# Optimization experiments

Measured on AMD Instinct MI355X. Metric: run time of the kernel, lower is better.

Reference implementation:

```python
import jax, jax.numpy as jnp
import numpy as np

NFEAT, NHID, NCLASS = 64, 64, 32
B, N_SOLUTE, N_SOLVENT = 2, 2076, 8940


def setup_inputs() -> dict:
    key = jax.random.key(0)
    ks = jax.random.split(key, 20)
    s = 0.05
    return {
        "solute_adj": jax.random.uniform(ks[0], (B, N_SOLUTE, N_SOLUTE), jnp.float32),
        "solute_meth": jax.random.normal(ks[1], (B, N_SOLUTE, NFEAT), jnp.float32),
        "solvent_meth": jax.random.normal(ks[2], (B, N_SOLVENT, NFEAT), jnp.float32),
        "solvent_adj_meth": jax.random.uniform(ks[3], (B, N_SOLVENT, N_SOLVENT), jnp.float32),
        "W_fc1": jax.random.normal(ks[4], (NFEAT, NCLASS), jnp.float32) * s,
        "b_fc1": jnp.zeros((NCLASS,), jnp.float32),
        "W_c1": jax.random.normal(ks[5], (NFEAT, NHID), jnp.float32) * s,
        "b_c1": jnp.zeros((NHID,), jnp.float32),
        "W_c2": jax.random.normal(ks[6], (NHID, NCLASS), jnp.float32) * s,
        "b_c2": jnp.zeros((NCLASS,), jnp.float32),
        "W_fc2": jax.random.normal(ks[7], (2 * NCLASS, NCLASS), jnp.float32) * s,
        "b_fc2": jnp.zeros((NCLASS,), jnp.float32),
        "W_fc3": jax.random.normal(ks[8], (NCLASS, 64), jnp.float32) * s,
        "b_fc3": jnp.zeros((64,), jnp.float32),
        "W_fc4": jax.random.normal(ks[9], (64, 32), jnp.float32) * s,
        "b_fc4": jnp.zeros((32,), jnp.float32),
        "W_fc5": jax.random.normal(ks[10], (32, 1), jnp.float32) * s,
        "b_fc5": jnp.zeros((1,), jnp.float32),
    }


def _branch(x, adj, W_fc1, b_fc1, W_c1, b_c1, W_c2, b_c2):
    # residual linear skip: fc1(x)
    init = x @ W_fc1 + b_fc1                          # [B, N, nclass]
    # GCNConv 1: adj @ (x W) + b, relu
    h = jax.nn.relu(jnp.einsum("bnm,bmh->bnh", adj, x @ W_c1) + b_c1)
    # GCNConv 2 + skip
    out = jnp.einsum("bnm,bmc->bnc", adj, h @ W_c2) + b_c2 + init  # [B, N, nclass]
    # global max pool: batch index is block-contiguous -> max over node axis
    return jnp.max(out, axis=1)                       # [B, nclass]


def reference(solute_adj, solute_meth, solvent_meth, solvent_adj_meth,
              W_fc1, b_fc1, W_c1, b_c1, W_c2, b_c2,
              W_fc2, b_fc2, W_fc3, b_fc3, W_fc4, b_fc4, W_fc5, b_fc5):
    su = _branch(solute_meth, solute_adj, W_fc1, b_fc1, W_c1, b_c1, W_c2, b_c2)
    sv = _branch(solvent_meth, solvent_adj_meth, W_fc1, b_fc1, W_c1, b_c1, W_c2, b_c2)
    d = jnp.concatenate([su, sv], axis=1)             # [B, 2*nclass]
    d = jax.nn.relu(d @ W_fc2 + b_fc2)                # dropout = identity (eval)
    d = jax.nn.relu(d @ W_fc3 + b_fc3)
    d = jax.nn.relu(d @ W_fc4 + b_fc4)
    return d @ W_fc5 + b_fc5                          # [B, 1]
```

## Files before the change

kernel.cpp:

```cpp
#include <hip/hip_runtime.h>

#define B_      2
#define NSU     2076
#define NSV     8940
#define ROWS_SU (B_ * NSU)
#define ROWS_ALL (B_ * (NSU + NSV))
#define NB64_SV 140
#define NB64_SU 33
#define NBX_TOT (2 * NB64_SV + 2 * NB64_SU)
#define NH2     8
#define NCH_SV  140
#define NCH_SU  33
#define TK_SV   140
#define TK_SU   33
#define T_SV    560
#define T_SU    132
#define TILES_TOT (2 * T_SV + 2 * T_SU)
#define PADROWS (TILES_TOT * 16)
#define TSZ8_SV ((size_t)140 * 1024)
#define TSZ8_SU ((size_t)34 * 1024)
#define SU_BASE8 ((size_t)2 * T_SV * TSZ8_SV)
#define PRE_BLKS ((ROWS_ALL + 255) / 256)
#define NEG_INF (-3.402823466e38f)

#define Y1F_SV(b) ((size_t)(b) * 140 * 4096)
#define Y1F_SU(b) ((size_t)2 * 140 * 4096 + (size_t)(b) * 34 * 4096)
#define Y2F8_SV(b) ((size_t)(b) * 140 * 2048)
#define Y2F8_SU(b) ((size_t)2 * 140 * 2048 + (size_t)(b) * 34 * 2048)

typedef __attribute__((ext_vector_type(8))) short bf16x8;
typedef __attribute__((ext_vector_type(4))) float f32x4;
typedef __attribute__((ext_vector_type(2))) long longx2;

#define MFMA16 __builtin_amdgcn_mfma_f32_16x16x32_bf16
#define MFMA8  __builtin_amdgcn_mfma_f32_16x16x32_fp8_fp8

__device__ __forceinline__ unsigned short f2bf(float x) {
    unsigned int u = __float_as_uint(x);
    u += 0x7FFFu + ((u >> 16) & 1u);
    return (unsigned short)(u >> 16);
}
__device__ __forceinline__ unsigned int pkbf(float lo, float hi) {
    unsigned int r;
    asm("v_cvt_pk_bf16_f32 %0, %1, %2" : "=v"(r) : "v"(lo), "v"(hi));
    return r;
}
__device__ __forceinline__ int pk8lo(float lo, float hi, int old) {
    return __builtin_amdgcn_cvt_pk_fp8_f32(lo, hi, old, false);
}
__device__ __forceinline__ int pk8hi(float lo, float hi, int old) {
    return __builtin_amdgcn_cvt_pk_fp8_f32(lo, hi, old, true);
}
__device__ __forceinline__ float bf2f(short s) {
    return __uint_as_float(((unsigned int)(unsigned short)s) << 16);
}

__global__ __launch_bounds__(256) void pre_kernel(
    const float* __restrict__ xsu, const float* __restrict__ xsv,
    const float* __restrict__ Wc1, const float* __restrict__ Wfc1,
    const float* __restrict__ bfc1, const float* __restrict__ Wc2g,
    unsigned short* __restrict__ y1tf, float* __restrict__ initb,
    unsigned short* __restrict__ wc2t)
{
    const int tid = threadIdx.x;
    if (blockIdx.x == PRE_BLKS) {
        for (int idx = tid; idx < 2048; idx += 256) {
            const int c = idx >> 6, f = idx & 63;
            wc2t[idx] = f2bf(Wc2g[f * 32 + c]);
        }
        return;
    }

    __shared__ float sWc1[64 * 64];
    __shared__ float sWfc1[64 * 32];
    __shared__ float sb[32];
    for (int i = tid; i < 64 * 64; i += 256) sWc1[i] = Wc1[i];
    for (int i = tid; i < 64 * 32; i += 256) sWfc1[i] = Wfc1[i];
    if (tid < 32) sb[tid] = bfc1[tid];
    __syncthreads();

    const int rid = blockIdx.x * 256 + tid;
    if (rid >= ROWS_ALL) return;

    const float* xrow; unsigned short* yb; int m;
    if (rid < ROWS_SU) {
        int b = rid / NSU; m = rid - b * NSU;
        xrow = xsu + (size_t)rid * 64;
        yb = y1tf + Y1F_SU(b);
    } else {
        int r2 = rid - ROWS_SU;
        int b = r2 / NSV; m = r2 - b * NSV;
        xrow = xsv + (size_t)r2 * 64;
        yb = y1tf + Y1F_SV(b);
    }

    float xr[64];
    #pragma unroll
    for (int f4 = 0; f4 < 16; ++f4) {
        float4 v = ((const float4*)xrow)[f4];
        xr[f4 * 4 + 0] = v.x; xr[f4 * 4 + 1] = v.y;
        xr[f4 * 4 + 2] = v.z; xr[f4 * 4 + 3] = v.w;
    }
    {
        const int chunk = m >> 6, half = (m >> 5) & 1, kqq = (m >> 3) & 3, e = m & 7;
        unsigned short* yw = yb + (size_t)chunk * 4096 + half * 512 + e;
        for (int c = 0; c < 64; ++c) {
            float acc = 0.f;
            #pragma unroll
            for (int f = 0; f < 64; ++f) acc += xr[f] * sWc1[f * 64 + c];
            yw[(c >> 4) * 1024 + ((c & 15) + 16 * kqq) * 8] = f2bf(acc);
        }
    }
    float* ini = initb + (size_t)rid * 32;
    for (int c = 0; c < 32; ++c) {
        float acc = sb[c];
        #pragma unroll
        for (int f = 0; f < 64; ++f) acc += xr[f] * sWfc1[f * 32 + c];
        ini[c] = acc;
    }
}

__global__ __launch_bounds__(256) void conv1f_kernel(
    const float* __restrict__ adj_su, const float* __restrict__ adj_sv,
    const unsigned short* __restrict__ y1tf,
    const float* __restrict__ bc1, const unsigned short* __restrict__ wc2t,
    unsigned char* __restrict__ abf8,
    unsigned char* __restrict__ y2f8)
{
    __shared__ unsigned short AL[4096];
    __shared__ unsigned short HL[1024];

    const int t = blockIdx.x;
    const int tid = threadIdx.x, lane = tid & 63, w = tid >> 6;
    const int l15 = lane & 15, kq = lane >> 4;

    int M, row0, TK;
    const float* A; const unsigned short* Yf;
    unsigned char* AbT; unsigned char* Y2b;
    if (t < 2 * T_SV) {
        int b = t / T_SV, rt = t - b * T_SV;
        M = NSV; TK = TK_SV;
        A = adj_sv + (size_t)b * NSV * NSV;
        Yf = y1tf + Y1F_SV(b);
        AbT = abf8 + (size_t)t * TSZ8_SV;
        Y2b = y2f8 + Y2F8_SV(b);
        row0 = rt * 16;
    } else {
        int u = t - 2 * T_SV;
        int b = u / T_SU, rt = u - b * T_SU;
        M = NSU; TK = TK_SU;
        A = adj_su + (size_t)b * NSU * NSU;
        Yf = y1tf + Y1F_SU(b);
        AbT = abf8 + SU_BASE8 + (size_t)u * TSZ8_SU;
        Y2b = y2f8 + Y2F8_SU(b);
        row0 = rt * 16;
    }

    const float* Ar[4];
    #pragma unroll
    for (int rr = 0; rr < 4; ++rr) {
        int r = row0 + w * 4 + rr;
        if (r >= M) r = M - 1;
        Ar[rr] = A + (size_t)r * M;
    }

    const int c4 = lane * 4;
    const int k64i = c4 >> 6;
    const int c63 = c4 & 63;
    const int rxor = (l15 & 7) << 3;

    f32x4 acc = {0.f, 0.f, 0.f, 0.f};

    for (int ch = 0; ch < TK; ch += 4) {
        const int cb = ch * 64;
        const int nk = (TK - ch < 4) ? (TK - ch) : 4;
        #pragma unroll
        for (int rr = 0; rr < 4; ++rr) {
            const int r = w * 4 + rr;
            const int col = cb + c4;
            float4 v = make_float4(0.f, 0.f, 0.f, 0.f);
            if (col < M) v = *(const float4*)(Ar[rr] + col);
            const unsigned int u0 = pkbf(v.x, v.y);
            const unsigned int u1 = pkbf(v.z, v.w);
            const int sa = k64i * 1024 + r * 64 + (c63 ^ ((r & 7) << 3));
            *(uint2*)(&AL[sa]) = make_uint2(u0, u1);
        }
        __syncthreads();
        #pragma unroll
        for (int j = 0; j < 4; ++j) {
            if (j < nk) {
                const bf16x8 af0 = *(const bf16x8*)(&AL[j * 1024 + l15 * 64 + ((kq * 8) ^ rxor)]);
                const bf16x8 af1 = *(const bf16x8*)(&AL[j * 1024 + l15 * 64 + ((32 + kq * 8) ^ rxor)]);
                const unsigned short* bb = Yf + (size_t)(ch + j) * 4096 + w * 1024 + lane * 8;
                const bf16x8 b0 = *(const bf16x8*)(bb);
                const bf16x8 b1 = *(const bf16x8*)(bb + 512);
                acc = MFMA16(af0, b0, acc, 0, 0, 0);
                acc = MFMA16(af1, b1, acc, 0, 0, 0);
            }
        }
        if (w < nk) {
            const bf16x8 h0 = *(const bf16x8*)(&AL[w * 1024 + l15 * 64 + ((kq * 8) ^ rxor)]);
            const bf16x8 h1 = *(const bf16x8*)(&AL[w * 1024 + l15 * 64 + ((32 + kq * 8) ^ rxor)]);
            int q0 = pk8lo(bf2f(h0[0]), bf2f(h0[1]), 0); q0 = pk8hi(bf2f(h0[2]), bf2f(h0[3]), q0);
            int q1 = pk8lo(bf2f(h0[4]), bf2f(h0[5]), 0); q1 = pk8hi(bf2f(h0[6]), bf2f(h0[7]), q1);
            int q2 = pk8lo(bf2f(h1[0]), bf2f(h1[1]), 0); q2 = pk8hi(bf2f(h1[2]), bf2f(h1[3]), q2);
            int q3 = pk8lo(bf2f(h1[4]), bf2f(h1[5]), 0); q3 = pk8hi(bf2f(h1[6]), bf2f(h1[7]), q3);
            *(int4*)(AbT + (size_t)(ch + w) * 1024 + lane * 16) = make_int4(q0, q1, q2, q3);
        }
        __syncthreads();
    }

    {
        const float bcv = bc1[w * 16 + l15];
        #pragma unroll
        for (int j = 0; j < 4; ++j) {
            const int r = kq * 4 + j;
            const int c = w * 16 + l15;
            HL[r * 64 + (c ^ ((r & 7) << 3))] = f2bf(fmaxf(acc[j] + bcv, 0.f));
        }
    }
    __syncthreads();
    if (w < 2) {
        const bf16x8 hf0 = *(const bf16x8*)(&HL[l15 * 64 + ((kq * 8) ^ rxor)]);
        const bf16x8 hf1 = *(const bf16x8*)(&HL[l15 * 64 + ((32 + kq * 8) ^ rxor)]);
        const unsigned short* wp = wc2t + (size_t)(w * 16 + l15) * 64 + kq * 8;
        const bf16x8 w0 = *(const bf16x8*)(wp);
        const bf16x8 w1 = *(const bf16x8*)(wp + 32);
        f32x4 m = {0.f, 0.f, 0.f, 0.f};
        m = MFMA16(hf0, w0, m, 0, 0, 0);
        m = MFMA16(hf1, w1, m, 0, 0, 0);
        const int mrow = row0 + kq * 4;
        const int chm = mrow >> 6, r6 = mrow & 63;
        const int halfm = r6 >> 5, kqqm = (r6 >> 3) & 3, e0 = r6 & 7;
        const int c = w * 16 + l15;
        int pk = pk8lo(m[0], m[1], 0); pk = pk8hi(m[2], m[3], pk);
        *(int*)(Y2b + (size_t)chm * 2048 + (c >> 4) * 1024
                + (kqqm * 16 + (c & 15)) * 16 + halfm * 8 + e0) = pk;
    }
}

__global__ __launch_bounds__(256) void conv2p_kernel(
    const unsigned char* __restrict__ abf8,
    const unsigned char* __restrict__ y2f8,
    float* __restrict__ p2)
{
    const int bid = (NBX_TOT - 1) - blockIdx.x;
    const int q = blockIdx.y;
    const int tid = threadIdx.x, lane = tid & 63, wid = tid >> 6;
    int tile0, cbeg, cend;
    const unsigned char* Yf2; const unsigned char* AbT;
    if (bid < 2 * NB64_SV) {
        int b = bid / NB64_SV, rb = bid - b * NB64_SV;
        Yf2 = y2f8 + Y2F8_SV(b);
        tile0 = b * T_SV + rb * 4;
        AbT = abf8 + (size_t)(tile0 + wid) * TSZ8_SV;
        cbeg = (q * NCH_SV) >> 3;
        cend = ((q + 1) * NCH_SV) >> 3;
    } else {
        int t = bid - 2 * NB64_SV;
        int b = t / NB64_SU, rb = t - b * NB64_SU;
        Yf2 = y2f8 + Y2F8_SU(b);
        int tsu = b * T_SU + rb * 4;
        tile0 = 2 * T_SV + tsu;
        AbT = abf8 + SU_BASE8 + (size_t)(tsu + wid) * TSZ8_SU;
        cbeg = (q * NCH_SU) >> 3;
        cend = ((q + 1) * NCH_SU) >> 3;
    }

    const int l15 = lane & 15, kq = lane >> 4;
    const unsigned char* Apl = AbT + (size_t)lane * 16;
    const unsigned char* Bpl = Yf2 + (size_t)lane * 16;

    f32x4 acc0 = {0.f,0.f,0.f,0.f}, acc1 = acc0;

    longx2 fa, fc;
    longx2 b0, b1, d0, d1;

#define LDA2(F, ch) do { F = *(const longx2*)(Apl + (size_t)(ch) * 1024); } while (0)
#define LDB2(B0,B1,ch) do { \
    const unsigned char* bb = Bpl + (size_t)(ch) * 2048; \
    B0 = *(const longx2*)(bb); \
    B1 = *(const longx2*)(bb + 1024); } while (0)
#define CMP4(F,B0,B1) do { \
    acc0 = MFMA8(F[0], B0[0], acc0, 0, 0, 0); \
    acc1 = MFMA8(F[0], B1[0], acc1, 0, 0, 0); \
    acc0 = MFMA8(F[1], B0[1], acc0, 0, 0, 0); \
    acc1 = MFMA8(F[1], B1[1], acc1, 0, 0, 0); } while (0)

    if (cbeg < cend) {
        LDA2(fa, cbeg);
        LDB2(b0, b1, cbeg);
        int ch = cbeg;
        while (ch + 2 <= cend) {
            LDA2(fc, ch + 1);
            LDB2(d0, d1, ch + 1);
            CMP4(fa, b0, b1);
            if (ch + 2 < cend) {
                LDA2(fa, ch + 2);
                LDB2(b0, b1, ch + 2);
            }
            CMP4(fc, d0, d1);
            ch += 2;
        }
        if (ch < cend) {
            CMP4(fa, b0, b1);
        }
    }
#undef LDA2
#undef LDB2
#undef CMP4

    float* Pp = p2 + ((size_t)q * TILES_TOT + tile0 + wid) * (16 * 32);
    #pragma unroll
    for (int j = 0; j < 4; ++j) {
        const int r = kq * 4 + j;
        Pp[r * 32 +      l15] = acc0[j];
        Pp[r * 32 + 16 + l15] = acc1[j];
    }
}

__global__ __launch_bounds__(256) void combine2_kernel(
    const float* __restrict__ p2, const float* __restrict__ bc2,
    const float* __restrict__ initb, float* __restrict__ part)
{
    const int idx = blockIdx.x * 256 + threadIdx.x;
    if (idx >= TILES_TOT * 32) return;
    const int gt = idx >> 5, c = idx & 31;
    int m0, M; const float* I;
    if (gt < 2 * T_SV) {
        int b = gt / T_SV;
        m0 = (gt - b * T_SV) * 16;
        M = NSV;
        I = initb + (size_t)ROWS_SU * 32 + (size_t)b * NSV * 32;
    } else {
        int t = gt - 2 * T_SV;
        int b = t / T_SU;
        m0 = (t - b * T_SU) * 16;
        M = NSU;
        I = initb + (size_t)b * NSU * 32;
    }
    const float* Q = p2 + (size_t)gt * 16 * 32 + c;
    const size_t QS = (size_t)TILES_TOT * 16 * 32;
    const float bb = bc2[c];
    float mx = NEG_INF;
    #pragma unroll
    for (int r = 0; r < 16; ++r) {
        const int m = m0 + r;
        if (m < M) {
            float s = bb + I[(size_t)m * 32 + c];
            #pragma unroll
            for (int qq = 0; qq < NH2; ++qq) s += Q[(size_t)qq * QS + r * 32];
            mx = fmaxf(mx, s);
        }
    }
    part[(size_t)gt * 32 + c] = mx;
}

__global__ __launch_bounds__(128) void head_kernel(
    const float* __restrict__ part,
    const float* __restrict__ Wfc2, const float* __restrict__ bfc2,
    const float* __restrict__ Wfc3, const float* __restrict__ bfc3,
    const float* __restrict__ Wfc4, const float* __restrict__ bfc4,
    const float* __restrict__ Wfc5, const float* __restrict__ bfc5,
    float* __restrict__ out)
{
    __shared__ float d[2][64];
    __shared__ float t1[2][32];
    __shared__ float t2[2][64];
    __shared__ float t3[2][32];
    const int tid = threadIdx.x;

    if (tid < 64) {
        const int b = tid >> 5, c = tid & 31;
        float m = NEG_INF;
        const float* ps = part + (size_t)(2 * T_SV + b * T_SU) * 32 + c;
        for (int i = 0; i < T_SU; ++i) m = fmaxf(m, ps[(size_t)i * 32]);
        d[b][c] = m;
        float m2 = NEG_INF;
        const float* pv = part + (size_t)b * T_SV * 32 + c;
        for (int i = 0; i < T_SV; ++i) m2 = fmaxf(m2, pv[(size_t)i * 32]);
        d[b][32 + c] = m2;
    }
    __syncthreads();
    if (tid < 64) {
        const int b = tid >> 5, c = tid & 31;
        float acc = bfc2[c];
        for (int f = 0; f < 64; ++f) acc += d[b][f] * Wfc2[f * 32 + c];
        t1[b][c] = fmaxf(acc, 0.f);
    }
    __syncthreads();
    {
        const int b = tid >> 6, c = tid & 63;
        float acc = bfc3[c];
        for (int f = 0; f < 32; ++f) acc += t1[b][f] * Wfc3[f * 64 + c];
        t2[b][c] = fmaxf(acc, 0.f);
    }
    __syncthreads();
    if (tid < 64) {
        const int b = tid >> 5, c = tid & 31;
        float acc = bfc4[c];
        for (int f = 0; f < 64; ++f) acc += t2[b][f] * Wfc4[f * 32 + c];
        t3[b][c] = fmaxf(acc, 0.f);
    }
    __syncthreads();
    if (tid < 2) {
        float acc = bfc5[0];
        for (int f = 0; f < 32; ++f) acc += t3[tid][f] * Wfc5[f];
        out[tid] = acc;
    }
}

extern "C" void kernel_launch(void* const* d_in, const int* in_sizes, int n_in,
                              void* d_out, int out_size, void* d_ws, size_t ws_size,
                              hipStream_t stream)
{
    const float* solute_adj   = (const float*)d_in[0];
    const float* solute_meth  = (const float*)d_in[1];
    const float* solvent_meth = (const float*)d_in[2];
    const float* solvent_adj  = (const float*)d_in[3];
    const float* W_fc1 = (const float*)d_in[4];
    const float* b_fc1 = (const float*)d_in[5];
    const float* W_c1  = (const float*)d_in[6];
    const float* b_c1  = (const float*)d_in[7];
    const float* W_c2  = (const float*)d_in[8];
    const float* b_c2  = (const float*)d_in[9];
    const float* W_fc2 = (const float*)d_in[10];
    const float* b_fc2 = (const float*)d_in[11];
    const float* W_fc3 = (const float*)d_in[12];
    const float* b_fc3 = (const float*)d_in[13];
    const float* W_fc4 = (const float*)d_in[14];
    const float* b_fc4 = (const float*)d_in[15];
    const float* W_fc5 = (const float*)d_in[16];
    const float* b_fc5 = (const float*)d_in[17];
    float* out = (float*)d_out;

    char* wsb = (char*)d_ws;
    size_t off = 0;
    unsigned short* y1tf = (unsigned short*)(wsb + off); off += 2850816;
    unsigned char*  y2f8 = (unsigned char*)(wsb + off);  off += 712704;
    unsigned short* wc2t = (unsigned short*)(wsb + off); off += 4096;
    float* initb         = (float*)(wsb + off);          off += 2820096;
    unsigned char* abf8  = (unsigned char*)(wsb + off);
    off += SU_BASE8 + (size_t)2 * T_SU * TSZ8_SU;
    off = (off + 15) & ~(size_t)15;
    float* p2            = (float*)(wsb + off);
    off += (size_t)NH2 * PADROWS * 32 * 4;
    float* part          = (float*)(wsb + off);          off += (size_t)TILES_TOT * 32 * 4;

    pre_kernel<<<dim3(PRE_BLKS + 1), dim3(256), 0, stream>>>(
        solute_meth, solvent_meth, W_c1, W_fc1, b_fc1, W_c2, y1tf, initb, wc2t);

    conv1f_kernel<<<dim3(TILES_TOT), dim3(256), 0, stream>>>(
        solute_adj, solvent_adj, y1tf, b_c1, wc2t, abf8, y2f8);

    conv2p_kernel<<<dim3(NBX_TOT, NH2), dim3(256), 0, stream>>>(abf8, y2f8, p2);

    combine2_kernel<<<dim3((TILES_TOT * 32 + 255) / 256), dim3(256), 0, stream>>>(
        p2, b_c2, initb, part);

    head_kernel<<<dim3(1), dim3(128), 0, stream>>>(
        part, W_fc2, b_fc2, W_fc3, b_fc3, W_fc4, b_fc4, W_fc5, b_fc5, out);
}
```

Baseline: 440.8 us.

## Double-buffer adjacency staging in conv1 and deepen conv2 fp8 load prefetch

```diff
diff --git a/kernel.cpp b/kernel.cpp
--- a/kernel.cpp
+++ b/kernel.cpp
@@ -127,7 +127,7 @@
     unsigned char* __restrict__ abf8,
     unsigned char* __restrict__ y2f8)
 {
-    __shared__ unsigned short AL[4096];
+    __shared__ unsigned short AL[2][4096];
     __shared__ unsigned short HL[1024];
 
     const int t = blockIdx.x;
@@ -170,46 +170,81 @@
     const int rxor = (l15 & 7) << 3;
 
     f32x4 acc = {0.f, 0.f, 0.f, 0.f};
-
-    for (int ch = 0; ch < TK; ch += 4) {
-        const int cb = ch * 64;
-        const int nk = (TK - ch < 4) ? (TK - ch) : 4;
-        #pragma unroll
-        for (int rr = 0; rr < 4; ++rr) {
-            const int r = w * 4 + rr;
-            const int col = cb + c4;
-            float4 v = make_float4(0.f, 0.f, 0.f, 0.f);
-            if (col < M) v = *(const float4*)(Ar[rr] + col);
-            const unsigned int u0 = pkbf(v.x, v.y);
-            const unsigned int u1 = pkbf(v.z, v.w);
-            const int sa = k64i * 1024 + r * 64 + (c63 ^ ((r & 7) << 3));
-            *(uint2*)(&AL[sa]) = make_uint2(u0, u1);
-        }
-        __syncthreads();
-        #pragma unroll
-        for (int j = 0; j < 4; ++j) {
-            if (j < nk) {
-                const bf16x8 af0 = *(const bf16x8*)(&AL[j * 1024 + l15 * 64 + ((kq * 8) ^ rxor)]);
-                const bf16x8 af1 = *(const bf16x8*)(&AL[j * 1024 + l15 * 64 + ((32 + kq * 8) ^ rxor)]);
-                const unsigned short* bb = Yf + (size_t)(ch + j) * 4096 + w * 1024 + lane * 8;
-                const bf16x8 b0 = *(const bf16x8*)(bb);
-                const bf16x8 b1 = *(const bf16x8*)(bb + 512);
-                acc = MFMA16(af0, b0, acc, 0, 0, 0);
-                acc = MFMA16(af1, b1, acc, 0, 0, 0);
-            }
-        }
-        if (w < nk) {
-            const bf16x8 h0 = *(const bf16x8*)(&AL[w * 1024 + l15 * 64 + ((kq * 8) ^ rxor)]);
-            const bf16x8 h1 = *(const bf16x8*)(&AL[w * 1024 + l15 * 64 + ((32 + kq * 8) ^ rxor)]);
-            int q0 = pk8lo(bf2f(h0[0]), bf2f(h0[1]), 0); q0 = pk8hi(bf2f(h0[2]), bf2f(h0[3]), q0);
-            int q1 = pk8lo(bf2f(h0[4]), bf2f(h0[5]), 0); q1 = pk8hi(bf2f(h0[6]), bf2f(h0[7]), q1);
-            int q2 = pk8lo(bf2f(h1[0]), bf2f(h1[1]), 0); q2 = pk8hi(bf2f(h1[2]), bf2f(h1[3]), q2);
-            int q3 = pk8lo(bf2f(h1[4]), bf2f(h1[5]), 0); q3 = pk8hi(bf2f(h1[6]), bf2f(h1[7]), q3);
-            *(int4*)(AbT + (size_t)(ch + w) * 1024 + lane * 16) = make_int4(q0, q1, q2, q3);
-        }
-        __syncthreads();
-    }
-
+    const int G = (TK + 3) >> 2;
+
+    float4 avA[4], avB[4];
+    #pragma unroll
+    for (int rr = 0; rr < 4; ++rr) {
+        float4 v = make_float4(0.f, 0.f, 0.f, 0.f);
+        if (c4 < M) v = *(const float4*)(Ar[rr] + c4);
+        avA[rr] = v;
+    }
+    #pragma unroll
+    for (int rr = 0; rr < 4; ++rr) {
+        const int col = 256 + c4;
+        float4 v = make_float4(0.f, 0.f, 0.f, 0.f);
+        if (G > 1 && col < M) v = *(const float4*)(Ar[rr] + col);
+        avB[rr] = v;
+    }
+
+#define ITER(AV, PARITY, gg) do { \
+    const int ch_ = (gg) * 4; \
+    const int nk_ = (TK - ch_ < 4) ? (TK - ch_) : 4; \
+    unsigned short* buf_ = &AL[PARITY][0]; \
+    _Pragma("unroll") \
+    for (int rr = 0; rr < 4; ++rr) { \
+        const int r_ = w * 4 + rr; \
+        const unsigned int u0_ = pkbf(AV[rr].x, AV[rr].y); \
+        const unsigned int u1_ = pkbf(AV[rr].z, AV[rr].w); \
+        const int sa_ = k64i * 1024 + r_ * 64 + (c63 ^ ((r_ & 7) << 3)); \
+        *(uint2*)(&buf_[sa_]) = make_uint2(u0_, u1_); \
+    } \
+    __syncthreads(); \
+    if ((gg) + 2 < G) { \
+        const int cb2_ = ((gg) + 2) * 256; \
+        _Pragma("unroll") \
+        for (int rr = 0; rr < 4; ++rr) { \
+            const int col_ = cb2_ + c4; \
+            float4 v_ = make_float4(0.f, 0.f, 0.f, 0.f); \
+            if (col_ < M) v_ = *(const float4*)(Ar[rr] + col_); \
+            AV[rr] = v_; \
+        } \
+    } \
+    _Pragma("unroll") \
+    for (int j = 0; j < 4; ++j) { \
+        if (j < nk_) { \
+            const bf16x8 af0_ = *(const bf16x8*)(&buf_[j * 1024 + l15 * 64 + ((kq * 8) ^ rxor)]); \
+            const bf16x8 af1_ = *(const bf16x8*)(&buf_[j * 1024 + l15 * 64 + ((32 + kq * 8) ^ rxor)]); \
+            const unsigned short* bb_ = Yf + (size_t)(ch_ + j) * 4096 + w * 1024 + lane * 8; \
+            const bf16x8 b0_ = *(const bf16x8*)(bb_); \
+            const bf16x8 b1_ = *(const bf16x8*)(bb_ + 512); \
+            acc = MFMA16(af0_, b0_, acc, 0, 0, 0); \
+            acc = MFMA16(af1_, b1_, acc, 0, 0, 0); \
+        } \
+    } \
+    if (w < nk_) { \
+        const bf16x8 h0_ = *(const bf16x8*)(&buf_[w * 1024 + l15 * 64 + ((kq * 8) ^ rxor)]); \
+        const bf16x8 h1_ = *(const bf16x8*)(&buf_[w * 1024 + l15 * 64 + ((32 + kq * 8) ^ rxor)]); \
+        int q0_ = pk8lo(bf2f(h0_[0]), bf2f(h0_[1]), 0); q0_ = pk8hi(bf2f(h0_[2]), bf2f(h0_[3]), q0_); \
+        int q1_ = pk8lo(bf2f(h0_[4]), bf2f(h0_[5]), 0); q1_ = pk8hi(bf2f(h0_[6]), bf2f(h0_[7]), q1_); \
+        int q2_ = pk8lo(bf2f(h1_[0]), bf2f(h1_[1]), 0); q2_ = pk8hi(bf2f(h1_[2]), bf2f(h1_[3]), q2_); \
+        int q3_ = pk8lo(bf2f(h1_[4]), bf2f(h1_[5]), 0); q3_ = pk8hi(bf2f(h1_[6]), bf2f(h1_[7]), q3_); \
+        *(int4*)(AbT + (size_t)(ch_ + w) * 1024 + lane * 16) = make_int4(q0_, q1_, q2_, q3_); \
+    } \
+} while (0)
+
+    int g = 0;
+    while (g < G) {
+        ITER(avA, 0, g);
+        ++g;
+        if (g < G) {
+            ITER(avB, 1, g);
+            ++g;
+        }
+    }
+#undef ITER
+
+    __syncthreads();
     {
         const float bcv = bc1[w * 16 + l15];
         #pragma unroll
@@ -273,14 +308,15 @@
 
     f32x4 acc0 = {0.f,0.f,0.f,0.f}, acc1 = acc0;
 
-    longx2 fa, fc;
-    longx2 b0, b1, d0, d1;
-
-#define LDA2(F, ch) do { F = *(const longx2*)(Apl + (size_t)(ch) * 1024); } while (0)
-#define LDB2(B0,B1,ch) do { \
-    const unsigned char* bb = Bpl + (size_t)(ch) * 2048; \
-    B0 = *(const longx2*)(bb); \
-    B1 = *(const longx2*)(bb + 1024); } while (0)
+    longx2 a0v, a1v, a2v, a3v;
+    longx2 b00, b01, b10, b11, b20, b21, b30, b31;
+
+#define LDSLOT(AV,B0,B1,ci) do { \
+    int cc_ = (ci); if (cc_ >= cend) cc_ = cend - 1; \
+    AV = *(const longx2*)(Apl + (size_t)cc_ * 1024); \
+    const unsigned char* bb_ = Bpl + (size_t)cc_ * 2048; \
+    B0 = *(const longx2*)(bb_); \
+    B1 = *(const longx2*)(bb_ + 1024); } while (0)
 #define CMP4(F,B0,B1) do { \
     acc0 = MFMA8(F[0], B0[0], acc0, 0, 0, 0); \
     acc1 = MFMA8(F[0], B1[0], acc1, 0, 0, 0); \
@@ -288,26 +324,24 @@
     acc1 = MFMA8(F[1], B1[1], acc1, 0, 0, 0); } while (0)
 
     if (cbeg < cend) {
-        LDA2(fa, cbeg);
-        LDB2(b0, b1, cbeg);
+        LDSLOT(a0v, b00, b01, cbeg);
+        LDSLOT(a1v, b10, b11, cbeg + 1);
+        LDSLOT(a2v, b20, b21, cbeg + 2);
+        LDSLOT(a3v, b30, b31, cbeg + 3);
         int ch = cbeg;
-        while (ch + 2 <= cend) {
-            LDA2(fc, ch + 1);
-            LDB2(d0, d1, ch + 1);
-            CMP4(fa, b0, b1);
-            if (ch + 2 < cend) {
-                LDA2(fa, ch + 2);
-                LDB2(b0, b1, ch + 2);
-            }
-            CMP4(fc, d0, d1);
-            ch += 2;
-        }
-        if (ch < cend) {
-            CMP4(fa, b0, b1);
-        }
-    }
-#undef LDA2
-#undef LDB2
+        while (ch + 4 <= cend) {
+            CMP4(a0v, b00, b01); LDSLOT(a0v, b00, b01, ch + 4);
+            CMP4(a1v, b10, b11); LDSLOT(a1v, b10, b11, ch + 5);
+            CMP4(a2v, b20, b21); LDSLOT(a2v, b20, b21, ch + 6);
+            CMP4(a3v, b30, b31); LDSLOT(a3v, b30, b31, ch + 7);
+            ch += 4;
+        }
+        if (ch     < cend) CMP4(a0v, b00, b01);
+        if (ch + 1 < cend) CMP4(a1v, b10, b11);
+        if (ch + 2 < cend) CMP4(a2v, b20, b21);
+        if (ch + 3 < cend) CMP4(a3v, b30, b31);
+    }
+#undef LDSLOT
 #undef CMP4
 
     float* Pp = p2 + ((size_t)q * TILES_TOT + tile0 + wid) * (16 * 32);
```

Result: faster. 414.0 us (-6.1%).
